# Kernel optimization log

Hardware: AMD Instinct MI355X
Metric: run time of the kernel (lower is better)

## Reference

```python
import jax, jax.numpy as jnp
import numpy as np

N_ATOMS = 2048
N_METAL = 512
BOX = (20.0, 20.0, 40.0)   # orthorhombic slab cell (A)
DL = 2.0                    # EwaldPotential dl -> k-grid half-extent per dim
SIGMA = 0.5540037           # 1/1.805132, Gaussian charge width
NMAX = tuple(int(np.ceil(L / DL)) for L in BOX)


def _kgrid():
    # integer reciprocal-lattice grid, k=0 excluded (built once at trace time)
    nx, ny, nz = NMAX
    g = np.stack(np.meshgrid(np.arange(-nx, nx + 1),
                             np.arange(-ny, ny + 1),
                             np.arange(-nz, nz + 1), indexing='ij'), -1).reshape(-1, 3)
    g = g[np.any(g != 0, axis=1)]
    return g.astype(np.float32)

_GRID = _kgrid()  # [K,3]


def ewald_field(r, q, cell):
    """Reciprocal-space Ewald potential phi_i = dE/dq_i for Gaussian-smeared charges.
    r:[N,3] q:[N,C] cell:[3,3] (rows = lattice vectors). Returns [N,C]."""
    V = jnp.abs(jnp.linalg.det(cell))
    recip = 2.0 * jnp.pi * jnp.linalg.inv(cell).T          # rows: reciprocal vectors
    k = jnp.asarray(_GRID, dtype=r.dtype) @ recip          # [K,3]
    k2 = jnp.sum(k * k, axis=-1)                           # [K]
    kfac = jnp.exp(-0.5 * SIGMA * SIGMA * k2) / k2         # exponent=1 kernel
    phase = r @ k.T                                        # [N,K]  (dominant traffic)
    c, s = jnp.cos(phase), jnp.sin(phase)
    cq = kfac[:, None] * (c.T @ q)                         # [K,C]
    sq = kfac[:, None] * (s.T @ q)
    return (4.0 * jnp.pi / V) * (c @ cq + s @ sq)          # [N,C]


def setup_inputs() -> dict:
    key = jax.random.key(0)
    k1, k2 = jax.random.split(key)
    box = jnp.asarray(BOX, dtype=jnp.float32)
    positions = jax.random.uniform(k1, (N_ATOMS, 3), dtype=jnp.float32) * box
    q = jax.random.normal(k2, (N_ATOMS, 1), dtype=jnp.float32) * 0.5
    cell = jnp.diag(box)
    # metal (Z=79) atoms occupy the first N_METAL slots; rest electrolyte (Z=8)
    atomic_numbers = jnp.concatenate([
        jnp.full((N_METAL,), 79, dtype=jnp.int32),
        jnp.full((N_ATOMS - N_METAL,), 8, dtype=jnp.int32)])
    return {"positions": positions, "q": q, "cell": cell,
            "atomic_numbers": atomic_numbers, "n_metal": N_METAL}


def reference(positions, q, cell, atomic_numbers, n_metal):
    nm = int(n_metal)  # static: metal atoms are the first nm rows
    dt = positions.dtype
    # q_all[metal] = 0
    q = q.at[:nm].set(0.0)
    # capacitance matrix S from detached coords (torch uses r.detach(), cell.detach())
    r_m = jax.lax.stop_gradient(positions[:nm])
    cell_d = jax.lax.stop_gradient(cell)
    A = ewald_field(r_m, jnp.eye(nm, dtype=dt), cell_d)     # [nm,nm] A_mat
    A_inv = jnp.linalg.inv(A)
    ones = jnp.ones((nm, 1), dtype=dt)
    Ai1 = A_inv @ ones                                       # [nm,1]
    S = A_inv - (Ai1 @ Ai1.T) / (ones.T @ Ai1)               # charge-neutral projector
    # full-system field; scaling_factor=1, external_field=None -> B_ext = 0
    f = ewald_field(positions, q, cell)                      # [N,1]
    B = -f[:nm]
    q_mw = q.at[:nm].set(S @ B)
    e_corr = jnp.zeros((1,), dtype=dt)   # scaling_factor == 1.0 branch
    e_ext = jnp.zeros((1,), dtype=dt)    # external_field is None
    return q_mw, e_corr, e_ext
```

## Files before the change

### kernel.cpp

```cpp
#include <hip/hip_runtime.h>
#include <math.h>

#define N_ATOMS 2048
#define NM      512
#define KHALF   9040
#define KPAD    9216
#define TWO_PI  6.2831853071795864769f
#define SIGMA   0.5540037f
#define FOUR_PI 12.566370614359172954f

__device__ inline void inv3x3(const float* __restrict__ c, float inv[3][3], float& det) {
    float a00=c[0],a01=c[1],a02=c[2],a10=c[3],a11=c[4],a12=c[5],a20=c[6],a21=c[7],a22=c[8];
    float c00 =  a11*a22 - a12*a21;
    float c01 = -(a10*a22 - a12*a20);
    float c02 =  a10*a21 - a11*a20;
    det = a00*c00 + a01*c01 + a02*c02;
    float id = 1.0f/det;
    inv[0][0] = c00*id;
    inv[0][1] = -(a01*a22 - a02*a21)*id;
    inv[0][2] =  (a01*a12 - a02*a11)*id;
    inv[1][0] = c01*id;
    inv[1][1] =  (a00*a22 - a02*a20)*id;
    inv[1][2] = -(a00*a12 - a02*a10)*id;
    inv[2][0] = c02*id;
// ... 22 lines not shown
                     float4* __restrict__ uq, float* __restrict__ out) {
    const int bb = blockIdx.x, tid = threadIdx.x;
    if (bb < 36) {
        int t = bb*256 + tid;
        float gx=0.f, gy=0.f, gz=0.f, wk=0.f;
        if (t < KHALF) {
            int iz = t % 41; int rem = t / 41; int iy = rem % 21; int ix = rem / 21;
            gx = (float)(ix - 10); gy = (float)(iy - 10); gz = (float)(iz - 20);
            float inv[3][3], det;
            inv3x3(cell, inv, det);
            float kx = TWO_PI*(gx*inv[0][0] + gy*inv[0][1] + gz*inv[0][2]);
            float ky = TWO_PI*(gx*inv[1][0] + gy*inv[1][1] + gz*inv[1][2]);
            float kz = TWO_PI*(gx*inv[2][0] + gy*inv[2][1] + gz*inv[2][2]);
            float k2 = kx*kx + ky*ky + kz*kz;
            float kfac = __expf(-0.5f*SIGMA*SIGMA*k2) / k2;
            wk = sqrtf(2.0f*kfac);
        }
        kdata[t] = make_float4(gx, gy, gz, wk);
    } else {
        int i = (bb-36)*256 + tid;
        float inv[3][3], det;
        inv3x3(cell, inv, det);
        float x = pos[3*i], y = pos[3*i+1], z = pos[3*i+2];
        float u = x*inv[0][0] + y*inv[1][0] + z*inv[2][0];
        float v = x*inv[0][1] + y*inv[1][1] + z*inv[2][1];
        float w = x*inv[0][2] + y*inv[1][2] + z*inv[2][2];
        float qi = qv[i];
        uq[i] = make_float4(u, v, w, qi);
        if (i >= NM) out[i] = qi;
        if (i == 0) { out[N_ATOMS] = 0.f; out[N_ATOMS+1] = 0.f; }
    }
}

__global__ void __launch_bounds__(256, 2) syrk_sf(const float4* __restrict__ kdata,
        const float4* __restrict__ uq, float* __restrict__ partial,
        float* __restrict__ Scw, float* __restrict__ Ssw, int SL, int KSL, int nsyrk) {
    __shared__ float smem[16384];
    const int tid = threadIdx.x;
    if ((int)blockIdx.x >= nsyrk) {
        int ch = blockIdx.x - nsyrk;
        int kk = tid & 63, sp = tid >> 6;
        int k = ch*64 + kk;
        float4 kd = kdata[k];
        float sc = 0.f, ss = 0.f;
        int jlo = NM + sp*384, jhi = jlo + 384;
        for (int j = jlo; j < jhi; ++j) {
            float4 at = uq[j];
            float ph = TWO_PI*(kd.x*at.x + kd.y*at.y + kd.z*at.z);
            float s, c; __sincosf(ph, &s, &c);
            sc += at.w * c;
            ss += at.w * s;
        }
        smem[sp*64 + kk] = sc;
        smem[256 + sp*64 + kk] = ss;
        __syncthreads();
        if (sp == 0) {
            float c = smem[kk] + smem[64+kk] + smem[128+kk] + smem[192+kk];
            float s = smem[256+kk] + smem[320+kk] + smem[384+kk] + smem[448+kk];
            float kf2 = kd.w * kd.w;
            Scw[k] = kf2 * c;
            Ssw[k] = kf2 * s;
        }
        return;
    }
    int s = blockIdx.x % SL;
    int t = blockIdx.x / SL;
    int rt = 0;
    while ((rt+1)*(rt+2)/2 <= t) ++rt;
    int ct = t - rt*(rt+1)/2;
    const int row0 = rt << 7, c0 = ct << 7;
    const bool diag = (row0 == c0);
    float* crT = smem; float* srT = smem+4096; float* ccT = smem+8192; float* scT = smem+12288;
    const float* ccR = diag ? crT : ccT;
    const float* scR = diag ? srT : scT;
    const int i0 = (tid & 15) << 3;
    const int j0 = (tid >> 4) << 3;
    float acc[8][8];
    #pragma unroll
    for (int i = 0; i < 8; ++i)
        #pragma unroll
        for (int j = 0; j < 8; ++j) acc[i][j] = 0.f;
    const int k0 = s * KSL;
    const int nch = KSL >> 5;
    for (int ch = 0; ch < nch; ++ch) {
        int kc = k0 + (ch << 5);
        __syncthreads();
        #pragma unroll
        for (int w = 0; w < 16; ++w) {
            int job = tid + (w << 8);
            int kk = job >> 7, a = job & 127;
            float4 kd = kdata[kc + kk];
            float4 at = uq[row0 + a];
            float ph = TWO_PI*(kd.x*at.x + kd.y*at.y + kd.z*at.z);
            float sn, cs;
            __sincosf(ph, &sn, &cs);
            crT[kk*128+a] = kd.w * cs;
            srT[kk*128+a] = kd.w * sn;
        }
        if (!diag) {
            #pragma unroll
            for (int w = 0; w < 16; ++w) {
                int job = tid + (w << 8);
                int kk = job >> 7, a = job & 127;
                float4 kd = kdata[kc + kk];
                float4 at = uq[c0 + a];
                float ph = TWO_PI*(kd.x*at.x + kd.y*at.y + kd.z*at.z);
                float sn, cs;
                __sincosf(ph, &sn, &cs);
                ccT[kk*128+a] = kd.w * cs;
                scT[kk*128+a] = kd.w * sn;
            }
        }
        __syncthreads();
        #pragma unroll 4
        for (int kk = 0; kk < 32; ++kk) {
            float cr[8], sr[8], cc[8], sv[8];
            *(float4*)&cr[0] = *(const float4*)&crT[kk*128+i0];
            *(float4*)&cr[4] = *(const float4*)&crT[kk*128+i0+4];
            *(float4*)&sr[0] = *(const float4*)&srT[kk*128+i0];
            *(float4*)&sr[4] = *(const float4*)&srT[kk*128+i0+4];
            *(float4*)&cc[0] = *(const float4*)&ccR[kk*128+j0];
            *(float4*)&cc[4] = *(const float4*)&ccR[kk*128+j0+4];
            *(float4*)&sv[0] = *(const float4*)&scR[kk*128+j0];
            *(float4*)&sv[4] = *(const float4*)&scR[kk*128+j0+4];
            #pragma unroll
            for (int i = 0; i < 8; ++i)
                #pragma unroll
                for (int j = 0; j < 8; ++j)
                    acc[i][j] += cr[i]*cc[j] + sr[i]*sv[j];
        }
    }
    float* P = partial + ((size_t)blockIdx.x << 14);
    #pragma unroll
    for (int i = 0; i < 8; ++i) {
        *(float4*)&P[(i0+i)*128 + j0]     = make_float4(acc[i][0], acc[i][1], acc[i][2], acc[i][3]);
        *(float4*)&P[(i0+i)*128 + j0 + 4] = make_float4(acc[i][4], acc[i][5], acc[i][6], acc[i][7]);
    }
}

__device__ void diag_fast(float* D, float* T, float* M, int tid, int pd, float* Dinvs) {
    __syncthreads();
    if (tid < 64) {
        float row[64];
        #pragma unroll
        for (int c = 0; c < 64; ++c) row[c] = D[tid*68 + c];
        #pragma unroll
        for (int j = 0; j < 64; ++j) {
            float pj = __shfl(row[j], j);
            float rinv = 1.0f / sqrtf(pj);
            float lj = row[j] * rinv;
            row[j] = lj;
            #pragma unroll
            for (int c = j+1; c < 64; ++c) {
                float lcj = __shfl(lj, c);
                row[c] = fmaf(-lj, lcj, row[c]);
            }
        }
        #pragma unroll
        for (int c = 0; c < 64; ++c) D[tid*68 + c] = row[c];
    }
    __syncthreads();
    for (int idx = tid; idx < 64*68; idx += 256) T[idx] = 0.f;
    __syncthreads();
    if (tid < 64) {
        int s = tid >> 3, c = tid & 7, o = s*8;
        float x[8];
        #pragma unroll
        for (int r = 0; r < 8; ++r) {
            float acc = (r == c) ? 1.0f : 0.0f;
// ... 67 lines not shown
                a0 += p[(size_t)(s+0) << 14];
                a1 += p[(size_t)(s+1) << 14];
                a2 += p[(size_t)(s+2) << 14];
                a3 += p[(size_t)(s+3) << 14];
                a4 += p[(size_t)(s+4) << 14];
                a5 += p[(size_t)(s+5) << 14];
                a6 += p[(size_t)(s+6) << 14];
                a7 += p[(size_t)(s+7) << 14];
            }
            for (; s < SL; ++s) a0 += p[(size_t)s << 14];
            float sum = ((a0+a1)+(a2+a3)) + ((a4+a5)+(a6+a7));
            float v = scal * sum;
            Amat[(size_t)i*512 + j] = v;
            Amat[(size_t)j*512 + i] = v;
        }
    } else {
        int ch = b - 512;
        int atom = ch*4 + (tid >> 6);
        int lane = tid & 63;
        float4 at = uq[atom];
        float acc = 0.f;
        for (int k = lane; k < KPAD; k += 64) {
            float4 kd = kdata[k];
            float ph = TWO_PI*(kd.x*at.x + kd.y*at.y + kd.z*at.z);
            float s, c; __sincosf(ph, &s, &c);
            acc += c*Scw[k] + s*Ssw[k];
        }
        #pragma unroll
        for (int off = 32; off; off >>= 1) acc += __shfl_down(acc, off);
        if (lane == 0) Bvec[atom] = -scal * acc;
    }
}

__global__ void __launch_bounds__(256) tail_chol(float* __restrict__ Amat,
        float* __restrict__ Lmat, float* __restrict__ LmatT, float* __restrict__ Dinvs,
        int* cnt, int* flag) {
    __shared__ float smem[15360];
    const int b = blockIdx.x, tid = threadIdx.x;
    const int G = 28;

    if (b == 0) {
        float* D = smem; float* T = smem + 4352; float* M = smem + 8704;
        for (int idx = tid; idx < 4096; idx += 256) {
            int r = idx >> 6, c = idx & 63;
            D[r*68+c] = Amat[(size_t)r*512 + c];
        }
        diag_fast(D, T, M, tid, 0, Dinvs);
    }
    gbar(cnt, flag, 1, G);

    for (int p = 0; p <= 6; ++p) {
        const int T7 = 7 - p, ntile = T7*(T7+1)/2;
        if (b < ntile) {
            const int tt = b;
            int rt = 0; while ((rt+1)*(rt+2)/2 <= tt) ++rt;
            const int ct = tt - rt*(rt+1)/2;
            const int R = p + 1 + rt, C = p + 1 + ct;
            float* ArT = smem;
            float* DvT = smem + 4352;
            float* LrT = smem + 8704;
            float* LcT = smem + 13056;
            float4 pref4[4];
            if (R != C) {
                #pragma unroll
                for (int w = 0; w < 4; ++w) {
                    int j = tid + (w << 8);
                    pref4[w] = *(const float4*)&Amat[(size_t)(C*64 + (j >> 4))*512 + p*64 + (j & 15)*4];
                }
            }
            __syncthreads();
            #pragma unroll
            for (int w = 0; w < 4; ++w) {
                int t4 = tid + (w << 8);
                float4 v = *(const float4*)&Dinvs[p*4096 + t4*4];
                int j = t4 >> 4, d0 = (t4 & 15)*4;
                DvT[(d0+0)*68 + j] = v.x;
                DvT[(d0+1)*68 + j] = v.y;
                DvT[(d0+2)*68 + j] = v.z;
                DvT[(d0+3)*68 + j] = v.w;
            }
            #pragma unroll
            for (int w = 0; w < 4; ++w) {
                int j = tid + (w << 8);
                int i = j >> 4, k0 = (j & 15)*4;
                float4 v = *(const float4*)&Amat[(size_t)(R*64 + i)*512 + p*64 + k0];
                ArT[(k0+0)*68 + i] = v.x;
                ArT[(k0+1)*68 + i] = v.y;
                ArT[(k0+2)*68 + i] = v.z;
                ArT[(k0+3)*68 + i] = v.w;
            }
            __syncthreads();
            const int i0 = (tid & 15)*4, j0 = (tid >> 4)*4;
            float lr[4][4];
            #pragma unroll
            for (int ii = 0; ii < 4; ++ii)
                #pragma unroll
                for (int jj = 0; jj < 4; ++jj) lr[ii][jj] = 0.f;
            for (int k = 0; k < 64; ++k) {
                float4 av = *(float4*)&ArT[k*68 + i0];
                float4 dv = *(float4*)&DvT[k*68 + j0];
                lr[0][0] += av.x*dv.x; lr[0][1] += av.x*dv.y; lr[0][2] += av.x*dv.z; lr[0][3] += av.x*dv.w;
                lr[1][0] += av.y*dv.x; lr[1][1] += av.y*dv.y; lr[1][2] += av.y*dv.z; lr[1][3] += av.y*dv.w;
                lr[2][0] += av.z*dv.x; lr[2][1] += av.z*dv.y; lr[2][2] += av.z*dv.z; lr[2][3] += av.z*dv.w;
                lr[3][0] += av.w*dv.x; lr[3][1] += av.w*dv.y; lr[3][2] += av.w*dv.z; lr[3][3] += av.w*dv.w;
            }
            #pragma unroll
            for (int ii = 0; ii < 4; ++ii)
                #pragma unroll
                for (int jj = 0; jj < 4; ++jj)
                    LrT[(j0+jj)*68 + i0+ii] = lr[ii][jj];
            __syncthreads();
            if (C == p + 1) {
                for (int idx = tid; idx < 4096; idx += 256) {
                    int i2 = idx >> 6, c2 = idx & 63;
                    Lmat[(size_t)(R*64+i2)*512 + p*64 + c2] = LrT[c2*68 + i2];
                }
                for (int idx = tid; idx < 4096; idx += 256) {
                    int c2 = idx >> 6, i2 = idx & 63;
                    LmatT[(size_t)(p*64+c2)*512 + R*64 + i2] = LrT[c2*68 + i2];
                }
            }
            if (R == C) {
                float up[4][4];
                #pragma unroll
                for (int ii = 0; ii < 4; ++ii)
                    #pragma unroll
                    for (int jj = 0; jj < 4; ++jj) up[ii][jj] = 0.f;
                for (int k = 0; k < 64; ++k) {
                    float4 av = *(float4*)&LrT[k*68 + i0];
                    float4 bv = *(float4*)&LrT[k*68 + j0];
                    up[0][0] += av.x*bv.x; up[0][1] += av.x*bv.y; up[0][2] += av.x*bv.z; up[0][3] += av.x*bv.w;
                    up[1][0] += av.y*bv.x; up[1][1] += av.y*bv.y; up[1][2] += av.y*bv.z; up[1][3] += av.y*bv.w;
                    up[2][0] += av.z*bv.x; up[2][1] += av.z*bv.y; up[2][2] += av.z*bv.z; up[2][3] += av.z*bv.w;
                    up[3][0] += av.w*bv.x; up[3][1] += av.w*bv.y; up[3][2] += av.w*bv.z; up[3][3] += av.w*bv.w;
                }
                float vals[4][4];
                #pragma unroll
                for (int ii = 0; ii < 4; ++ii)
                    #pragma unroll
                    for (int jj = 0; jj < 4; ++jj) {
                        size_t gix = (size_t)(R*64+i0+ii)*512 + C*64 + j0 + jj;
                        float v = Amat[gix] - up[ii][jj];
                        Amat[gix] = v;
                        vals[ii][jj] = v;
                    }
                if (tt == 0) {
                    float* D = smem; float* T = smem + 4352; float* M = smem + 8704;
                    __syncthreads();
                    #pragma unroll
                    for (int ii = 0; ii < 4; ++ii)
                        #pragma unroll
                        for (int jj = 0; jj < 4; ++jj)
                            D[(i0+ii)*68 + j0+jj] = vals[ii][jj];
                    diag_fast(D, T, M, tid, p+1, Dinvs);
                }
            } else {
                #pragma unroll
                for (int w = 0; w < 4; ++w) {
                    int j = tid + (w << 8);
                    int i = j >> 4, k0 = (j & 15)*4;
                    ArT[(k0+0)*68 + i] = pref4[w].x;
                    ArT[(k0+1)*68 + i] = pref4[w].y;
                    ArT[(k0+2)*68 + i] = pref4[w].z;
                    ArT[(k0+3)*68 + i] = pref4[w].w;
                }
                __syncthreads();
                const int c0l = (tid & 15)*4, jr0 = (tid >> 4)*2;
                #pragma unroll
                for (int hh = 0; hh < 2; ++hh) {
                    float lc[4][2];
                    #pragma unroll
                    for (int cc = 0; cc < 4; ++cc) { lc[cc][0] = 0.f; lc[cc][1] = 0.f; }
                    for (int d = 0; d < 64; ++d) {
                        float4 dv = *(float4*)&DvT[d*68 + c0l];
                        float2 av = *(float2*)&ArT[d*68 + hh*32 + jr0];
                        lc[0][0] += dv.x*av.x; lc[0][1] += dv.x*av.y;
                        lc[1][0] += dv.y*av.x; lc[1][1] += dv.y*av.y;
                        lc[2][0] += dv.z*av.x; lc[2][1] += dv.z*av.y;
                        lc[3][0] += dv.w*av.x; lc[3][1] += dv.w*av.y;
                    }
                    __syncthreads();
                    #pragma unroll
                    for (int cc = 0; cc < 4; ++cc) {
                        LcT[(c0l+cc)*36 + jr0]     = lc[cc][0];
                        LcT[(c0l+cc)*36 + jr0 + 1] = lc[cc][1];
                    }
                    __syncthreads();
                    float up[4][2];
                    #pragma unroll
                    for (int ii = 0; ii < 4; ++ii) { up[ii][0] = 0.f; up[ii][1] = 0.f; }
                    for (int c2 = 0; c2 < 64; ++c2) {
                        float4 lv = *(float4*)&LrT[c2*68 + i0];
                        float2 cv = *(float2*)&LcT[c2*36 + jr0];
                        up[0][0] += lv.x*cv.x; up[0][1] += lv.x*cv.y;
                        up[1][0] += lv.y*cv.x; up[1][1] += lv.y*cv.y;
                        up[2][0] += lv.z*cv.x; up[2][1] += lv.z*cv.y;
                        up[3][0] += lv.w*cv.x; up[3][1] += lv.w*cv.y;
                    }
                    #pragma unroll
                    for (int ii = 0; ii < 4; ++ii)
                        #pragma unroll
                        for (int jr = 0; jr < 2; ++jr) {
                            size_t gix = (size_t)(R*64+i0+ii)*512 + C*64 + hh*32 + jr0 + jr;
                            Amat[gix] -= up[ii][jr];
                        }
                }
            }
        }
        if (p < 6) gbar(cnt, flag, p + 2, G);
    }
}

__global__ void __launch_bounds__(512) solve(const float* __restrict__ Lmat,
        const float* __restrict__ LmatT, const float* __restrict__ Dinvs,
        const float* __restrict__ Bvec, float* __restrict__ out) {
    __shared__ float smem[2592];
    float* rb  = smem;
    float* ro  = smem + 512;
    float* xb  = smem + 1024;
    float* xo  = smem + 1536;
    float* bvs = smem + 2048;
    float* red = smem + 2560;
    const int tid = threadIdx.x;
    if (tid < 512) {
        float bv = Bvec[tid];
        bvs[tid] = bv; rb[tid] = bv; ro[tid] = 1.0f;
    }
    __syncthreads();
    for (int k = 0; k < 8; ++k) {
        if (tid < 64) {
            const float* Dk = Dinvs + k*4096 + tid*64;
            float s1 = 0.f, s2 = 0.f;
            for (int c4 = 0; c4 < 16; ++c4) {
                float4 w = *(const float4*)&Dk[c4*4];
                int cb = 64*k + c4*4;
                s1 += w.x*rb[cb] + w.y*rb[cb+1] + w.z*rb[cb+2] + w.w*rb[cb+3];
                s2 += w.x*ro[cb] + w.y*ro[cb+1] + w.z*ro[cb+2] + w.w*ro[cb+3];
            }
            rb[64*k+tid] = s1; ro[64*k+tid] = s2;
        }
        __syncthreads();
        for (int mm = 64*(k+1) + tid; mm < 512; mm += 512) {
// ... 44 lines not shown
        #pragma unroll
        for (int i = 0; i < 8; ++i) { sn += red[i]; sd += red[16+i]; }
        red[31] = sn / sd;
    }
    __syncthreads();
    float ratio = red[31];
    if (tid < 512) out[tid] = xb[tid] - xo[tid]*ratio;
}

extern "C" void kernel_launch(void* const* d_in, const int* in_sizes, int n_in,
                              void* d_out, int out_size, void* d_ws, size_t ws_size,
                              hipStream_t stream) {
    (void)in_sizes; (void)n_in; (void)out_size;
    const float* pos  = (const float*)d_in[0];
    const float* qv   = (const float*)d_in[1];
    const float* cell = (const float*)d_in[2];
    float* out = (float*)d_out;
    char* ws = (char*)d_ws;
    size_t off = 0;
    auto alloc = [&](size_t bytes) -> void* {
        void* p = (void*)(ws + off);
        off = (off + bytes + 255) & ~(size_t)255;
        return p;
    };
    float4* kdata = (float4*)alloc((size_t)KPAD*16);
    float4* uq    = (float4*)alloc((size_t)N_ATOMS*16);
    float*  Scw   = (float*)alloc((size_t)KPAD*4);
    float*  Ssw   = (float*)alloc((size_t)KPAD*4);
    float*  Bvec  = (float*)alloc(512*4);
    float*  Amat  = (float*)alloc((size_t)512*512*4);
    float*  Lmat  = (float*)alloc((size_t)512*512*4);
    float*  LmatT = (float*)alloc((size_t)512*512*4);
    float*  Dinvs = (float*)alloc((size_t)8*4096*4);
    int* bar = (int*)alloc(256);
    static const int slopts[10] = {96, 72, 48, 36, 24, 16, 12, 8, 4, 1};
    int SL = 1;
    for (int ci = 0; ci < 10; ++ci) {
        size_t need = (size_t)10 * slopts[ci] * 16384 * 4;
        if (off + need <= ws_size) { SL = slopts[ci]; break; }
    }
    float* partial = (float*)alloc((size_t)10*SL*16384*4);
    const int KSL = KPAD / SL;
    const int nsyrk = 10*SL;

    hipMemsetAsync(bar, 0, 8, stream);
    prep<<<dim3(44), dim3(256), 0, stream>>>(pos, qv, cell, kdata, uq, out);
    syrk_sf<<<dim3(nsyrk + 144), dim3(256), 0, stream>>>(kdata, uq, partial,
                                                         Scw, Ssw, SL, KSL, nsyrk);
    redfield<<<dim3(640), dim3(256), 0, stream>>>(partial, cell, Amat, kdata, uq,
                                                  Scw, Ssw, Bvec, SL);
    tail_chol<<<dim3(28), dim3(256), 0, stream>>>(Amat, Lmat, LmatT, Dinvs,
                                                  bar, bar + 1);
    solve<<<dim3(1), dim3(512), 0, stream>>>(Lmat, LmatT, Dinvs, Bvec, out);
}
```

Measured before the change: 537.5 us.

## Serialize last Cholesky panels in one block and interleave GEMM thread tiles

The per-tile Cholesky update is factored into a helper. The blocked Cholesky now runs only the first four panel steps across the cooperative grid with global barriers. The last three steps, which have few tiles, run sequentially in block 0 after a single arrival counter, so several grid-wide barriers are removed in exchange for serial work on one block. Separately, the Ewald GEMM thread mapping changes from contiguous 8x8 sub-tiles to two 4-wide groups strided by 64, which is meant to reduce LDS bank conflicts on the float4 loads.

```diff
diff --git a/kernel.cpp b/kernel.cpp
--- a/kernel.cpp
+++ b/kernel.cpp
@@ -119,8 +119,8 @@
     float* crT = smem; float* srT = smem+4096; float* ccT = smem+8192; float* scT = smem+12288;
     const float* ccR = diag ? crT : ccT;
     const float* scR = diag ? srT : scT;
-    const int i0 = (tid & 15) << 3;
-    const int j0 = (tid >> 4) << 3;
+    const int i0 = (tid & 15) << 2;
+    const int j0 = (tid >> 4) << 2;
     float acc[8][8];
     #pragma unroll
     for (int i = 0; i < 8; ++i)
@@ -160,15 +160,18 @@
         __syncthreads();
         #pragma unroll 4
         for (int kk = 0; kk < 32; ++kk) {
-            float cr[8], sr[8], cc[8], sv[8];
-            *(float4*)&cr[0] = *(const float4*)&crT[kk*128+i0];
-            *(float4*)&cr[4] = *(const float4*)&crT[kk*128+i0+4];
-            *(float4*)&sr[0] = *(const float4*)&srT[kk*128+i0];
-            *(float4*)&sr[4] = *(const float4*)&srT[kk*128+i0+4];
-            *(float4*)&cc[0] = *(const float4*)&ccR[kk*128+j0];
-            *(float4*)&cc[4] = *(const float4*)&ccR[kk*128+j0+4];
-            *(float4*)&sv[0] = *(const float4*)&scR[kk*128+j0];
-            *(float4*)&sv[4] = *(const float4*)&scR[kk*128+j0+4];
+            float4 c0v = *(const float4*)&crT[kk*128+i0];
+            float4 c1v = *(const float4*)&crT[kk*128+i0+64];
+            float4 s0v = *(const float4*)&srT[kk*128+i0];
+            float4 s1v = *(const float4*)&srT[kk*128+i0+64];
+            float4 d0v = *(const float4*)&ccR[kk*128+j0];
+            float4 d1v = *(const float4*)&ccR[kk*128+j0+64];
+            float4 t0v = *(const float4*)&scR[kk*128+j0];
+            float4 t1v = *(const float4*)&scR[kk*128+j0+64];
+            float cr[8] = {c0v.x,c0v.y,c0v.z,c0v.w, c1v.x,c1v.y,c1v.z,c1v.w};
+            float sr[8] = {s0v.x,s0v.y,s0v.z,s0v.w, s1v.x,s1v.y,s1v.z,s1v.w};
+            float cc[8] = {d0v.x,d0v.y,d0v.z,d0v.w, d1v.x,d1v.y,d1v.z,d1v.w};
+            float sv[8] = {t0v.x,t0v.y,t0v.z,t0v.w, t1v.x,t1v.y,t1v.z,t1v.w};
             #pragma unroll
             for (int i = 0; i < 8; ++i)
                 #pragma unroll
@@ -179,8 +182,9 @@
     float* P = partial + ((size_t)blockIdx.x << 14);
     #pragma unroll
     for (int i = 0; i < 8; ++i) {
-        *(float4*)&P[(i0+i)*128 + j0]     = make_float4(acc[i][0], acc[i][1], acc[i][2], acc[i][3]);
-        *(float4*)&P[(i0+i)*128 + j0 + 4] = make_float4(acc[i][4], acc[i][5], acc[i][6], acc[i][7]);
+        int row = (i < 4) ? (i0 + i) : (64 + i0 + i - 4);
+        *(float4*)&P[row*128 + j0]      = make_float4(acc[i][0], acc[i][1], acc[i][2], acc[i][3]);
+        *(float4*)&P[row*128 + j0 + 64] = make_float4(acc[i][4], acc[i][5], acc[i][6], acc[i][7]);
     }
 }
 
@@ -314,6 +318,163 @@
     }
 }
 
+__device__ void chol_tile(float* Amat, float* Lmat, float* LmatT, float* Dinvs,
+                          float* smem, int tid, int p, int tt) {
+    int rt = 0; while ((rt+1)*(rt+2)/2 <= tt) ++rt;
+    const int ct = tt - rt*(rt+1)/2;
+    const int R = p + 1 + rt, C = p + 1 + ct;
+    float* ArT = smem;
+    float* DvT = smem + 4352;
+    float* LrT = smem + 8704;
+    float* LcT = smem + 13056;
+    float4 pref4[4];
+    if (R != C) {
+        #pragma unroll
+        for (int w = 0; w < 4; ++w) {
+            int j = tid + (w << 8);
+            pref4[w] = *(const float4*)&Amat[(size_t)(C*64 + (j >> 4))*512 + p*64 + (j & 15)*4];
+        }
+    }
+    __syncthreads();
+    #pragma unroll
+    for (int w = 0; w < 4; ++w) {
+        int t4 = tid + (w << 8);
+        float4 v = *(const float4*)&Dinvs[p*4096 + t4*4];
+        int j = t4 >> 4, d0 = (t4 & 15)*4;
+        DvT[(d0+0)*68 + j] = v.x;
+        DvT[(d0+1)*68 + j] = v.y;
+        DvT[(d0+2)*68 + j] = v.z;
+        DvT[(d0+3)*68 + j] = v.w;
+    }
+    #pragma unroll
+    for (int w = 0; w < 4; ++w) {
+        int j = tid + (w << 8);
+        int i = j >> 4, k0 = (j & 15)*4;
+        float4 v = *(const float4*)&Amat[(size_t)(R*64 + i)*512 + p*64 + k0];
+        ArT[(k0+0)*68 + i] = v.x;
+        ArT[(k0+1)*68 + i] = v.y;
+        ArT[(k0+2)*68 + i] = v.z;
+        ArT[(k0+3)*68 + i] = v.w;
+    }
+    __syncthreads();
+    const int i0 = (tid & 15)*4, j0 = (tid >> 4)*4;
+    float lr[4][4];
+    #pragma unroll
+    for (int ii = 0; ii < 4; ++ii)
+        #pragma unroll
+        for (int jj = 0; jj < 4; ++jj) lr[ii][jj] = 0.f;
+    for (int k = 0; k < 64; ++k) {
+        float4 av = *(float4*)&ArT[k*68 + i0];
+        float4 dv = *(float4*)&DvT[k*68 + j0];
+        lr[0][0] += av.x*dv.x; lr[0][1] += av.x*dv.y; lr[0][2] += av.x*dv.z; lr[0][3] += av.x*dv.w;
+        lr[1][0] += av.y*dv.x; lr[1][1] += av.y*dv.y; lr[1][2] += av.y*dv.z; lr[1][3] += av.y*dv.w;
+        lr[2][0] += av.z*dv.x; lr[2][1] += av.z*dv.y; lr[2][2] += av.z*dv.z; lr[2][3] += av.z*dv.w;
+        lr[3][0] += av.w*dv.x; lr[3][1] += av.w*dv.y; lr[3][2] += av.w*dv.z; lr[3][3] += av.w*dv.w;
+    }
+    #pragma unroll
+    for (int ii = 0; ii < 4; ++ii)
+        #pragma unroll
+        for (int jj = 0; jj < 4; ++jj)
+            LrT[(j0+jj)*68 + i0+ii] = lr[ii][jj];
+    __syncthreads();
+    if (C == p + 1) {
+        for (int idx = tid; idx < 4096; idx += 256) {
+            int i2 = idx >> 6, c2 = idx & 63;
+            Lmat[(size_t)(R*64+i2)*512 + p*64 + c2] = LrT[c2*68 + i2];
+        }
+        for (int idx = tid; idx < 4096; idx += 256) {
+            int c2 = idx >> 6, i2 = idx & 63;
+            LmatT[(size_t)(p*64+c2)*512 + R*64 + i2] = LrT[c2*68 + i2];
+        }
+    }
+    if (R == C) {
+        float up[4][4];
+        #pragma unroll
+        for (int ii = 0; ii < 4; ++ii)
+            #pragma unroll
+            for (int jj = 0; jj < 4; ++jj) up[ii][jj] = 0.f;
+        for (int k = 0; k < 64; ++k) {
+            float4 av = *(float4*)&LrT[k*68 + i0];
+            float4 bv = *(float4*)&LrT[k*68 + j0];
+            up[0][0] += av.x*bv.x; up[0][1] += av.x*bv.y; up[0][2] += av.x*bv.z; up[0][3] += av.x*bv.w;
+            up[1][0] += av.y*bv.x; up[1][1] += av.y*bv.y; up[1][2] += av.y*bv.z; up[1][3] += av.y*bv.w;
+            up[2][0] += av.z*bv.x; up[2][1] += av.z*bv.y; up[2][2] += av.z*bv.z; up[2][3] += av.z*bv.w;
+            up[3][0] += av.w*bv.x; up[3][1] += av.w*bv.y; up[3][2] += av.w*bv.z; up[3][3] += av.w*bv.w;
+        }
+        float vals[4][4];
+        #pragma unroll
+        for (int ii = 0; ii < 4; ++ii)
+            #pragma unroll
+            for (int jj = 0; jj < 4; ++jj) {
+                size_t gix = (size_t)(R*64+i0+ii)*512 + C*64 + j0 + jj;
+                float v = Amat[gix] - up[ii][jj];
+                Amat[gix] = v;
+                vals[ii][jj] = v;
+            }
+        if (tt == 0) {
+            float* D = smem; float* T = smem + 4352; float* M = smem + 8704;
+            __syncthreads();
+            #pragma unroll
+            for (int ii = 0; ii < 4; ++ii)
+                #pragma unroll
+                for (int jj = 0; jj < 4; ++jj)
+                    D[(i0+ii)*68 + j0+jj] = vals[ii][jj];
+            diag_fast(D, T, M, tid, p+1, Dinvs);
+        }
+    } else {
+        #pragma unroll
+        for (int w = 0; w < 4; ++w) {
+            int j = tid + (w << 8);
+            int i = j >> 4, k0 = (j & 15)*4;
+            ArT[(k0+0)*68 + i] = pref4[w].x;
+            ArT[(k0+1)*68 + i] = pref4[w].y;
+            ArT[(k0+2)*68 + i] = pref4[w].z;
+            ArT[(k0+3)*68 + i] = pref4[w].w;
+        }
+        __syncthreads();
+        const int c0l = (tid & 15)*4, jr0 = (tid >> 4)*2;
+        #pragma unroll
+        for (int hh = 0; hh < 2; ++hh) {
+            float lc[4][2];
+            #pragma unroll
+            for (int cc = 0; cc < 4; ++cc) { lc[cc][0] = 0.f; lc[cc][1] = 0.f; }
+            for (int d = 0; d < 64; ++d) {
+                float4 dv = *(float4*)&DvT[d*68 + c0l];
+                float2 av = *(float2*)&ArT[d*68 + hh*32 + jr0];
+                lc[0][0] += dv.x*av.x; lc[0][1] += dv.x*av.y;
+                lc[1][0] += dv.y*av.x; lc[1][1] += dv.y*av.y;
+                lc[2][0] += dv.z*av.x; lc[2][1] += dv.z*av.y;
+                lc[3][0] += dv.w*av.x; lc[3][1] += dv.w*av.y;
+            }
+            __syncthreads();
+            #pragma unroll
+            for (int cc = 0; cc < 4; ++cc) {
+                LcT[(c0l+cc)*36 + jr0]     = lc[cc][0];
+                LcT[(c0l+cc)*36 + jr0 + 1] = lc[cc][1];
+            }
+            __syncthreads();
+            float up[4][2];
+            #pragma unroll
+            for (int ii = 0; ii < 4; ++ii) { up[ii][0] = 0.f; up[ii][1] = 0.f; }
+            for (int c2 = 0; c2 < 64; ++c2) {
+                float4 lv = *(float4*)&LrT[c2*68 + i0];
+                float2 cv = *(float2*)&LcT[c2*36 + jr0];
+                up[0][0] += lv.x*cv.x; up[0][1] += lv.x*cv.y;
+                up[1][0] += lv.y*cv.x; up[1][1] += lv.y*cv.y;
+                up[2][0] += lv.z*cv.x; up[2][1] += lv.z*cv.y;
+                up[3][0] += lv.w*cv.x; up[3][1] += lv.w*cv.y;
+            }
+            #pragma unroll
+            for (int ii = 0; ii < 4; ++ii)
+                #pragma unroll
+                for (int jr = 0; jr < 2; ++jr) {
+                    size_t gix = (size_t)(R*64+i0+ii)*512 + C*64 + hh*32 + jr0 + jr;
+                    Amat[gix] -= up[ii][jr];
+                }
+        }
+    }
+}
+
 __global__ void __launch_bounds__(256) tail_chol(float* __restrict__ Amat,
         float* __restrict__ Lmat, float* __restrict__ LmatT, float* __restrict__ Dinvs,
         int* cnt, int* flag) {
@@ -331,165 +492,25 @@
     }
     gbar(cnt, flag, 1, G);
 
-    for (int p = 0; p <= 6; ++p) {
+    for (int p = 0; p <= 3; ++p) {
         const int T7 = 7 - p, ntile = T7*(T7+1)/2;
-        if (b < ntile) {
-            const int tt = b;
-            int rt = 0; while ((rt+1)*(rt+2)/2 <= tt) ++rt;
-            const int ct = tt - rt*(rt+1)/2;
-            const int R = p + 1 + rt, C = p + 1 + ct;
-            float* ArT = smem;
-            float* DvT = smem + 4352;
-            float* LrT = smem + 8704;
-            float* LcT = smem + 13056;
-            float4 pref4[4];
-            if (R != C) {
-                #pragma unroll
-                for (int w = 0; w < 4; ++w) {
-                    int j = tid + (w << 8);
-                    pref4[w] = *(const float4*)&Amat[(size_t)(C*64 + (j >> 4))*512 + p*64 + (j & 15)*4];
-                }
-            }
-            __syncthreads();
-            #pragma unroll
-            for (int w = 0; w < 4; ++w) {
-                int t4 = tid + (w << 8);
-                float4 v = *(const float4*)&Dinvs[p*4096 + t4*4];
-                int j = t4 >> 4, d0 = (t4 & 15)*4;
-                DvT[(d0+0)*68 + j] = v.x;
-                DvT[(d0+1)*68 + j] = v.y;
-                DvT[(d0+2)*68 + j] = v.z;
-                DvT[(d0+3)*68 + j] = v.w;
-            }
-            #pragma unroll
-            for (int w = 0; w < 4; ++w) {
-                int j = tid + (w << 8);
-                int i = j >> 4, k0 = (j & 15)*4;
-                float4 v = *(const float4*)&Amat[(size_t)(R*64 + i)*512 + p*64 + k0];
-                ArT[(k0+0)*68 + i] = v.x;
-                ArT[(k0+1)*68 + i] = v.y;
-                ArT[(k0+2)*68 + i] = v.z;
-                ArT[(k0+3)*68 + i] = v.w;
-            }
-            __syncthreads();
-            const int i0 = (tid & 15)*4, j0 = (tid >> 4)*4;
-            float lr[4][4];
-            #pragma unroll
-            for (int ii = 0; ii < 4; ++ii)
-                #pragma unroll
-                for (int jj = 0; jj < 4; ++jj) lr[ii][jj] = 0.f;
-            for (int k = 0; k < 64; ++k) {
-                float4 av = *(float4*)&ArT[k*68 + i0];
-                float4 dv = *(float4*)&DvT[k*68 + j0];
-                lr[0][0] += av.x*dv.x; lr[0][1] += av.x*dv.y; lr[0][2] += av.x*dv.z; lr[0][3] += av.x*dv.w;
-                lr[1][0] += av.y*dv.x; lr[1][1] += av.y*dv.y; lr[1][2] += av.y*dv.z; lr[1][3] += av.y*dv.w;
-                lr[2][0] += av.z*dv.x; lr[2][1] += av.z*dv.y; lr[2][2] += av.z*dv.z; lr[2][3] += av.z*dv.w;
-                lr[3][0] += av.w*dv.x; lr[3][1] += av.w*dv.y; lr[3][2] += av.w*dv.z; lr[3][3] += av.w*dv.w;
-            }
-            #pragma unroll
-            for (int ii = 0; ii < 4; ++ii)
-                #pragma unroll
-                for (int jj = 0; jj < 4; ++jj)
-                    LrT[(j0+jj)*68 + i0+ii] = lr[ii][jj];
-            __syncthreads();
-            if (C == p + 1) {
-                for (int idx = tid; idx < 4096; idx += 256) {
-                    int i2 = idx >> 6, c2 = idx & 63;
-                    Lmat[(size_t)(R*64+i2)*512 + p*64 + c2] = LrT[c2*68 + i2];
-                }
-                for (int idx = tid; idx < 4096; idx += 256) {
-                    int c2 = idx >> 6, i2 = idx & 63;
-                    LmatT[(size_t)(p*64+c2)*512 + R*64 + i2] = LrT[c2*68 + i2];
-                }
-            }
-            if (R == C) {
-                float up[4][4];
-                #pragma unroll
-                for (int ii = 0; ii < 4; ++ii)
-                    #pragma unroll
-                    for (int jj = 0; jj < 4; ++jj) up[ii][jj] = 0.f;
-                for (int k = 0; k < 64; ++k) {
-                    float4 av = *(float4*)&LrT[k*68 + i0];
-                    float4 bv = *(float4*)&LrT[k*68 + j0];
-                    up[0][0] += av.x*bv.x; up[0][1] += av.x*bv.y; up[0][2] += av.x*bv.z; up[0][3] += av.x*bv.w;
-                    up[1][0] += av.y*bv.x; up[1][1] += av.y*bv.y; up[1][2] += av.y*bv.z; up[1][3] += av.y*bv.w;
-                    up[2][0] += av.z*bv.x; up[2][1] += av.z*bv.y; up[2][2] += av.z*bv.z; up[2][3] += av.z*bv.w;
-                    up[3][0] += av.w*bv.x; up[3][1] += av.w*bv.y; up[3][2] += av.w*bv.z; up[3][3] += av.w*bv.w;
-                }
-                float vals[4][4];
-                #pragma unroll
-                for (int ii = 0; ii < 4; ++ii)
-                    #pragma unroll
-                    for (int jj = 0; jj < 4; ++jj) {
-                        size_t gix = (size_t)(R*64+i0+ii)*512 + C*64 + j0 + jj;
-                        float v = Amat[gix] - up[ii][jj];
-                        Amat[gix] = v;
-                        vals[ii][jj] = v;
-                    }
-                if (tt == 0) {
-                    float* D = smem; float* T = smem + 4352; float* M = smem + 8704;
-                    __syncthreads();
-                    #pragma unroll
-                    for (int ii = 0; ii < 4; ++ii)
-                        #pragma unroll
-                        for (int jj = 0; jj < 4; ++jj)
-                            D[(i0+ii)*68 + j0+jj] = vals[ii][jj];
-                    diag_fast(D, T, M, tid, p+1, Dinvs);
-                }
-            } else {
-                #pragma unroll
-                for (int w = 0; w < 4; ++w) {
-                    int j = tid + (w << 8);
-                    int i = j >> 4, k0 = (j & 15)*4;
-                    ArT[(k0+0)*68 + i] = pref4[w].x;
-                    ArT[(k0+1)*68 + i] = pref4[w].y;
-                    ArT[(k0+2)*68 + i] = pref4[w].z;
-                    ArT[(k0+3)*68 + i] = pref4[w].w;
-                }
-                __syncthreads();
-                const int c0l = (tid & 15)*4, jr0 = (tid >> 4)*2;
-                #pragma unroll
-                for (int hh = 0; hh < 2; ++hh) {
-                    float lc[4][2];
-                    #pragma unroll
-                    for (int cc = 0; cc < 4; ++cc) { lc[cc][0] = 0.f; lc[cc][1] = 0.f; }
-                    for (int d = 0; d < 64; ++d) {
-                        float4 dv = *(float4*)&DvT[d*68 + c0l];
-                        float2 av = *(float2*)&ArT[d*68 + hh*32 + jr0];
-                        lc[0][0] += dv.x*av.x; lc[0][1] += dv.x*av.y;
-                        lc[1][0] += dv.y*av.x; lc[1][1] += dv.y*av.y;
-                        lc[2][0] += dv.z*av.x; lc[2][1] += dv.z*av.y;
-                        lc[3][0] += dv.w*av.x; lc[3][1] += dv.w*av.y;
-                    }
-                    __syncthreads();
-                    #pragma unroll
-                    for (int cc = 0; cc < 4; ++cc) {
-                        LcT[(c0l+cc)*36 + jr0]     = lc[cc][0];
-                        LcT[(c0l+cc)*36 + jr0 + 1] = lc[cc][1];
-                    }
-                    __syncthreads();
-                    float up[4][2];
-                    #pragma unroll
-                    for (int ii = 0; ii < 4; ++ii) { up[ii][0] = 0.f; up[ii][1] = 0.f; }
-                    for (int c2 = 0; c2 < 64; ++c2) {
-                        float4 lv = *(float4*)&LrT[c2*68 + i0];
-                        float2 cv = *(float2*)&LcT[c2*36 + jr0];
-                        up[0][0] += lv.x*cv.x; up[0][1] += lv.x*cv.y;
-                        up[1][0] += lv.y*cv.x; up[1][1] += lv.y*cv.y;
-                        up[2][0] += lv.z*cv.x; up[2][1] += lv.z*cv.y;
-                        up[3][0] += lv.w*cv.x; up[3][1] += lv.w*cv.y;
-                    }
-                    #pragma unroll
-                    for (int ii = 0; ii < 4; ++ii)
-                        #pragma unroll
-                        for (int jr = 0; jr < 2; ++jr) {
-                            size_t gix = (size_t)(R*64+i0+ii)*512 + C*64 + hh*32 + jr0 + jr;
-                            Amat[gix] -= up[ii][jr];
-                        }
-                }
-            }
-        }
-        if (p < 6) gbar(cnt, flag, p + 2, G);
+        if (b < ntile) chol_tile(Amat, Lmat, LmatT, Dinvs, smem, tid, p, b);
+        if (p < 3) gbar(cnt, flag, p + 2, G);
+    }
+    __syncthreads();
+    if (tid == 0)
+        __hip_atomic_fetch_add(cnt, 1, __ATOMIC_RELEASE, __HIP_MEMORY_SCOPE_AGENT);
+    if (b != 0) return;
+    if (tid == 0) {
+        while (__hip_atomic_load(cnt, __ATOMIC_RELAXED, __HIP_MEMORY_SCOPE_AGENT) < G*5)
+            __builtin_amdgcn_s_sleep(2);
+        (void)__hip_atomic_load(cnt, __ATOMIC_ACQUIRE, __HIP_MEMORY_SCOPE_AGENT);
+    }
+    __syncthreads();
+    for (int p = 4; p <= 6; ++p) {
+        const int T7 = 7 - p, ntile = T7*(T7+1)/2;
+        for (int tt = 0; tt < ntile; ++tt)
+            chol_tile(Amat, Lmat, LmatT, Dinvs, smem, tid, p, tt);
     }
 }
 
```

Measured after the change: 631.9 us. 17.6% more time.

## Precompute weighted cos/sin table once instead of recomputing per SYRK tile

Applied to the files above, without the earlier changes.

Adds a kernel that writes a weighted cos/sin table of shape [K,512] for the metal atoms into two ~19 MB global buffers. The SYRK blocks then load their tiles from this table with float4 loads instead of recomputing sincos for every (row, column) tile pair, which removes redundant transcendental work repeated across the 10 tile pairs. In exchange it adds about 38 MB of write and read traffic, and the workspace gets smaller, which may force a lower SL split. The Cholesky tile body is also moved into a device function with no change in behaviour.

```diff
diff --git a/kernel.cpp b/kernel.cpp
--- a/kernel.cpp
+++ b/kernel.cpp
@@ -78,8 +78,40 @@
     }
 }
 
+__global__ void __launch_bounds__(256) tabk(const float4* __restrict__ kdata,
+        const float4* __restrict__ uq, float* __restrict__ Tc, float* __restrict__ Ts) {
+    int e = blockIdx.x*256 + threadIdx.x;
+    int k = e >> 7;
+    int a0 = (e & 127) << 2;
+    float4 kd = kdata[k];
+    float4 cs4, sn4;
+    {
+        float4 at = uq[a0+0];
+        float ph = TWO_PI*(kd.x*at.x + kd.y*at.y + kd.z*at.z);
+        float s, c; __sincosf(ph, &s, &c); cs4.x = kd.w*c; sn4.x = kd.w*s;
+    }
+    {
+        float4 at = uq[a0+1];
+        float ph = TWO_PI*(kd.x*at.x + kd.y*at.y + kd.z*at.z);
+        float s, c; __sincosf(ph, &s, &c); cs4.y = kd.w*c; sn4.y = kd.w*s;
+    }
+    {
+        float4 at = uq[a0+2];
+        float ph = TWO_PI*(kd.x*at.x + kd.y*at.y + kd.z*at.z);
+        float s, c; __sincosf(ph, &s, &c); cs4.z = kd.w*c; sn4.z = kd.w*s;
+    }
+    {
+        float4 at = uq[a0+3];
+        float ph = TWO_PI*(kd.x*at.x + kd.y*at.y + kd.z*at.z);
+        float s, c; __sincosf(ph, &s, &c); cs4.w = kd.w*c; sn4.w = kd.w*s;
+    }
+    *(float4*)&Tc[(size_t)k*512 + a0] = cs4;
+    *(float4*)&Ts[(size_t)k*512 + a0] = sn4;
+}
+
 __global__ void __launch_bounds__(256, 2) syrk_sf(const float4* __restrict__ kdata,
-        const float4* __restrict__ uq, float* __restrict__ partial,
+        const float4* __restrict__ uq, const float* __restrict__ Tc,
+        const float* __restrict__ Ts, float* __restrict__ partial,
         float* __restrict__ Scw, float* __restrict__ Ssw, int SL, int KSL, int nsyrk) {
     __shared__ float smem[16384];
     const int tid = threadIdx.x;
@@ -132,29 +164,21 @@
         int kc = k0 + (ch << 5);
         __syncthreads();
         #pragma unroll
-        for (int w = 0; w < 16; ++w) {
-            int job = tid + (w << 8);
-            int kk = job >> 7, a = job & 127;
-            float4 kd = kdata[kc + kk];
-            float4 at = uq[row0 + a];
-            float ph = TWO_PI*(kd.x*at.x + kd.y*at.y + kd.z*at.z);
-            float sn, cs;
-            __sincosf(ph, &sn, &cs);
-            crT[kk*128+a] = kd.w * cs;
-            srT[kk*128+a] = kd.w * sn;
+        for (int w = 0; w < 4; ++w) {
+            int e = tid + (w << 8);
+            int kk = e >> 5, a4 = (e & 31) << 2;
+            size_t gix = (size_t)(kc + kk)*512 + row0 + a4;
+            *(float4*)&crT[kk*128 + a4] = *(const float4*)&Tc[gix];
+            *(float4*)&srT[kk*128 + a4] = *(const float4*)&Ts[gix];
         }
         if (!diag) {
             #pragma unroll
-            for (int w = 0; w < 16; ++w) {
-                int job = tid + (w << 8);
-                int kk = job >> 7, a = job & 127;
-                float4 kd = kdata[kc + kk];
-                float4 at = uq[c0 + a];
-                float ph = TWO_PI*(kd.x*at.x + kd.y*at.y + kd.z*at.z);
-                float sn, cs;
-                __sincosf(ph, &sn, &cs);
-                ccT[kk*128+a] = kd.w * cs;
-                scT[kk*128+a] = kd.w * sn;
+            for (int w = 0; w < 4; ++w) {
+                int e = tid + (w << 8);
+                int kk = e >> 5, a4 = (e & 31) << 2;
+                size_t gix = (size_t)(kc + kk)*512 + c0 + a4;
+                *(float4*)&ccT[kk*128 + a4] = *(const float4*)&Tc[gix];
+                *(float4*)&scT[kk*128 + a4] = *(const float4*)&Ts[gix];
             }
         }
         __syncthreads();
@@ -314,6 +338,163 @@
     }
 }
 
+__device__ void chol_tile(float* Amat, float* Lmat, float* LmatT, float* Dinvs,
+                          float* smem, int tid, int p, int tt) {
+    int rt = 0; while ((rt+1)*(rt+2)/2 <= tt) ++rt;
+    const int ct = tt - rt*(rt+1)/2;
+    const int R = p + 1 + rt, C = p + 1 + ct;
+    float* ArT = smem;
+    float* DvT = smem + 4352;
+    float* LrT = smem + 8704;
+    float* LcT = smem + 13056;
+    float4 pref4[4];
+    if (R != C) {
+        #pragma unroll
+        for (int w = 0; w < 4; ++w) {
+            int j = tid + (w << 8);
+            pref4[w] = *(const float4*)&Amat[(size_t)(C*64 + (j >> 4))*512 + p*64 + (j & 15)*4];
+        }
+    }
+    __syncthreads();
+    #pragma unroll
+    for (int w = 0; w < 4; ++w) {
+        int t4 = tid + (w << 8);
+        float4 v = *(const float4*)&Dinvs[p*4096 + t4*4];
+        int j = t4 >> 4, d0 = (t4 & 15)*4;
+        DvT[(d0+0)*68 + j] = v.x;
+        DvT[(d0+1)*68 + j] = v.y;
+        DvT[(d0+2)*68 + j] = v.z;
+        DvT[(d0+3)*68 + j] = v.w;
+    }
+    #pragma unroll
+    for (int w = 0; w < 4; ++w) {
+        int j = tid + (w << 8);
+        int i = j >> 4, k0 = (j & 15)*4;
+        float4 v = *(const float4*)&Amat[(size_t)(R*64 + i)*512 + p*64 + k0];
+        ArT[(k0+0)*68 + i] = v.x;
+        ArT[(k0+1)*68 + i] = v.y;
+        ArT[(k0+2)*68 + i] = v.z;
+        ArT[(k0+3)*68 + i] = v.w;
+    }
+    __syncthreads();
+    const int i0 = (tid & 15)*4, j0 = (tid >> 4)*4;
+    float lr[4][4];
+    #pragma unroll
+    for (int ii = 0; ii < 4; ++ii)
+        #pragma unroll
+        for (int jj = 0; jj < 4; ++jj) lr[ii][jj] = 0.f;
+    for (int k = 0; k < 64; ++k) {
+        float4 av = *(float4*)&ArT[k*68 + i0];
+        float4 dv = *(float4*)&DvT[k*68 + j0];
+        lr[0][0] += av.x*dv.x; lr[0][1] += av.x*dv.y; lr[0][2] += av.x*dv.z; lr[0][3] += av.x*dv.w;
+        lr[1][0] += av.y*dv.x; lr[1][1] += av.y*dv.y; lr[1][2] += av.y*dv.z; lr[1][3] += av.y*dv.w;
+        lr[2][0] += av.z*dv.x; lr[2][1] += av.z*dv.y; lr[2][2] += av.z*dv.z; lr[2][3] += av.z*dv.w;
+        lr[3][0] += av.w*dv.x; lr[3][1] += av.w*dv.y; lr[3][2] += av.w*dv.z; lr[3][3] += av.w*dv.w;
+    }
+    #pragma unroll
+    for (int ii = 0; ii < 4; ++ii)
+        #pragma unroll
+        for (int jj = 0; jj < 4; ++jj)
+            LrT[(j0+jj)*68 + i0+ii] = lr[ii][jj];
+    __syncthreads();
+    if (C == p + 1) {
+        for (int idx = tid; idx < 4096; idx += 256) {
+            int i2 = idx >> 6, c2 = idx & 63;
+            Lmat[(size_t)(R*64+i2)*512 + p*64 + c2] = LrT[c2*68 + i2];
+        }
+        for (int idx = tid; idx < 4096; idx += 256) {
+            int c2 = idx >> 6, i2 = idx & 63;
+            LmatT[(size_t)(p*64+c2)*512 + R*64 + i2] = LrT[c2*68 + i2];
+        }
+    }
+    if (R == C) {
+        float up[4][4];
+        #pragma unroll
+        for (int ii = 0; ii < 4; ++ii)
+            #pragma unroll
+            for (int jj = 0; jj < 4; ++jj) up[ii][jj] = 0.f;
+        for (int k = 0; k < 64; ++k) {
+            float4 av = *(float4*)&LrT[k*68 + i0];
+            float4 bv = *(float4*)&LrT[k*68 + j0];
+            up[0][0] += av.x*bv.x; up[0][1] += av.x*bv.y; up[0][2] += av.x*bv.z; up[0][3] += av.x*bv.w;
+            up[1][0] += av.y*bv.x; up[1][1] += av.y*bv.y; up[1][2] += av.y*bv.z; up[1][3] += av.y*bv.w;
+            up[2][0] += av.z*bv.x; up[2][1] += av.z*bv.y; up[2][2] += av.z*bv.z; up[2][3] += av.z*bv.w;
+            up[3][0] += av.w*bv.x; up[3][1] += av.w*bv.y; up[3][2] += av.w*bv.z; up[3][3] += av.w*bv.w;
+        }
+        float vals[4][4];
+        #pragma unroll
+        for (int ii = 0; ii < 4; ++ii)
+            #pragma unroll
+            for (int jj = 0; jj < 4; ++jj) {
+                size_t gix = (size_t)(R*64+i0+ii)*512 + C*64 + j0 + jj;
+                float v = Amat[gix] - up[ii][jj];
+                Amat[gix] = v;
+                vals[ii][jj] = v;
+            }
+        if (tt == 0) {
+            float* D = smem; float* T = smem + 4352; float* M = smem + 8704;
+            __syncthreads();
+            #pragma unroll
+            for (int ii = 0; ii < 4; ++ii)
+                #pragma unroll
+                for (int jj = 0; jj < 4; ++jj)
+                    D[(i0+ii)*68 + j0+jj] = vals[ii][jj];
+            diag_fast(D, T, M, tid, p+1, Dinvs);
+        }
+    } else {
+        #pragma unroll
+        for (int w = 0; w < 4; ++w) {
+            int j = tid + (w << 8);
+            int i = j >> 4, k0 = (j & 15)*4;
+            ArT[(k0+0)*68 + i] = pref4[w].x;
+            ArT[(k0+1)*68 + i] = pref4[w].y;
+            ArT[(k0+2)*68 + i] = pref4[w].z;
+            ArT[(k0+3)*68 + i] = pref4[w].w;
+        }
+        __syncthreads();
+        const int c0l = (tid & 15)*4, jr0 = (tid >> 4)*2;
+        #pragma unroll
+        for (int hh = 0; hh < 2; ++hh) {
+            float lc[4][2];
+            #pragma unroll
+            for (int cc = 0; cc < 4; ++cc) { lc[cc][0] = 0.f; lc[cc][1] = 0.f; }
+            for (int d = 0; d < 64; ++d) {
+                float4 dv = *(float4*)&DvT[d*68 + c0l];
+                float2 av = *(float2*)&ArT[d*68 + hh*32 + jr0];
+                lc[0][0] += dv.x*av.x; lc[0][1] += dv.x*av.y;
+                lc[1][0] += dv.y*av.x; lc[1][1] += dv.y*av.y;
+                lc[2][0] += dv.z*av.x; lc[2][1] += dv.z*av.y;
+                lc[3][0] += dv.w*av.x; lc[3][1] += dv.w*av.y;
+            }
+            __syncthreads();
+            #pragma unroll
+            for (int cc = 0; cc < 4; ++cc) {
+                LcT[(c0l+cc)*36 + jr0]     = lc[cc][0];
+                LcT[(c0l+cc)*36 + jr0 + 1] = lc[cc][1];
+            }
+            __syncthreads();
+            float up[4][2];
+            #pragma unroll
+            for (int ii = 0; ii < 4; ++ii) { up[ii][0] = 0.f; up[ii][1] = 0.f; }
+            for (int c2 = 0; c2 < 64; ++c2) {
+                float4 lv = *(float4*)&LrT[c2*68 + i0];
+                float2 cv = *(float2*)&LcT[c2*36 + jr0];
+                up[0][0] += lv.x*cv.x; up[0][1] += lv.x*cv.y;
+                up[1][0] += lv.y*cv.x; up[1][1] += lv.y*cv.y;
+                up[2][0] += lv.z*cv.x; up[2][1] += lv.z*cv.y;
+                up[3][0] += lv.w*cv.x; up[3][1] += lv.w*cv.y;
+            }
+            #pragma unroll
+            for (int ii = 0; ii < 4; ++ii)
+                #pragma unroll
+                for (int jr = 0; jr < 2; ++jr) {
+                    size_t gix = (size_t)(R*64+i0+ii)*512 + C*64 + hh*32 + jr0 + jr;
+                    Amat[gix] -= up[ii][jr];
+                }
+        }
+    }
+}
+
 __global__ void __launch_bounds__(256) tail_chol(float* __restrict__ Amat,
         float* __restrict__ Lmat, float* __restrict__ LmatT, float* __restrict__ Dinvs,
         int* cnt, int* flag) {
@@ -333,162 +514,7 @@
 
     for (int p = 0; p <= 6; ++p) {
         const int T7 = 7 - p, ntile = T7*(T7+1)/2;
-        if (b < ntile) {
-            const int tt = b;
-            int rt = 0; while ((rt+1)*(rt+2)/2 <= tt) ++rt;
-            const int ct = tt - rt*(rt+1)/2;
-            const int R = p + 1 + rt, C = p + 1 + ct;
-            float* ArT = smem;
-            float* DvT = smem + 4352;
-            float* LrT = smem + 8704;
-            float* LcT = smem + 13056;
-            float4 pref4[4];
-            if (R != C) {
-                #pragma unroll
-                for (int w = 0; w < 4; ++w) {
-                    int j = tid + (w << 8);
-                    pref4[w] = *(const float4*)&Amat[(size_t)(C*64 + (j >> 4))*512 + p*64 + (j & 15)*4];
-                }
-            }
-            __syncthreads();
-            #pragma unroll
-            for (int w = 0; w < 4; ++w) {
-                int t4 = tid + (w << 8);
-                float4 v = *(const float4*)&Dinvs[p*4096 + t4*4];
-                int j = t4 >> 4, d0 = (t4 & 15)*4;
-                DvT[(d0+0)*68 + j] = v.x;
-                DvT[(d0+1)*68 + j] = v.y;
-                DvT[(d0+2)*68 + j] = v.z;
-                DvT[(d0+3)*68 + j] = v.w;
-            }
-            #pragma unroll
-            for (int w = 0; w < 4; ++w) {
-                int j = tid + (w << 8);
-                int i = j >> 4, k0 = (j & 15)*4;
-                float4 v = *(const float4*)&Amat[(size_t)(R*64 + i)*512 + p*64 + k0];
-                ArT[(k0+0)*68 + i] = v.x;
-                ArT[(k0+1)*68 + i] = v.y;
-                ArT[(k0+2)*68 + i] = v.z;
-                ArT[(k0+3)*68 + i] = v.w;
-            }
-            __syncthreads();
-            const int i0 = (tid & 15)*4, j0 = (tid >> 4)*4;
-            float lr[4][4];
-            #pragma unroll
-            for (int ii = 0; ii < 4; ++ii)
-                #pragma unroll
-                for (int jj = 0; jj < 4; ++jj) lr[ii][jj] = 0.f;
-            for (int k = 0; k < 64; ++k) {
-                float4 av = *(float4*)&ArT[k*68 + i0];
-                float4 dv = *(float4*)&DvT[k*68 + j0];
-                lr[0][0] += av.x*dv.x; lr[0][1] += av.x*dv.y; lr[0][2] += av.x*dv.z; lr[0][3] += av.x*dv.w;
-                lr[1][0] += av.y*dv.x; lr[1][1] += av.y*dv.y; lr[1][2] += av.y*dv.z; lr[1][3] += av.y*dv.w;
-                lr[2][0] += av.z*dv.x; lr[2][1] += av.z*dv.y; lr[2][2] += av.z*dv.z; lr[2][3] += av.z*dv.w;
-                lr[3][0] += av.w*dv.x; lr[3][1] += av.w*dv.y; lr[3][2] += av.w*dv.z; lr[3][3] += av.w*dv.w;
-            }
-            #pragma unroll
-            for (int ii = 0; ii < 4; ++ii)
-                #pragma unroll
-                for (int jj = 0; jj < 4; ++jj)
-                    LrT[(j0+jj)*68 + i0+ii] = lr[ii][jj];
-            __syncthreads();
-            if (C == p + 1) {
-                for (int idx = tid; idx < 4096; idx += 256) {
-                    int i2 = idx >> 6, c2 = idx & 63;
-                    Lmat[(size_t)(R*64+i2)*512 + p*64 + c2] = LrT[c2*68 + i2];
-                }
-                for (int idx = tid; idx < 4096; idx += 256) {
-                    int c2 = idx >> 6, i2 = idx & 63;
-                    LmatT[(size_t)(p*64+c2)*512 + R*64 + i2] = LrT[c2*68 + i2];
-                }
-            }
-            if (R == C) {
-                float up[4][4];
-                #pragma unroll
-                for (int ii = 0; ii < 4; ++ii)
-                    #pragma unroll
-                    for (int jj = 0; jj < 4; ++jj) up[ii][jj] = 0.f;
-                for (int k = 0; k < 64; ++k) {
-                    float4 av = *(float4*)&LrT[k*68 + i0];
-                    float4 bv = *(float4*)&LrT[k*68 + j0];
-                    up[0][0] += av.x*bv.x; up[0][1] += av.x*bv.y; up[0][2] += av.x*bv.z; up[0][3] += av.x*bv.w;
-                    up[1][0] += av.y*bv.x; up[1][1] += av.y*bv.y; up[1][2] += av.y*bv.z; up[1][3] += av.y*bv.w;
-                    up[2][0] += av.z*bv.x; up[2][1] += av.z*bv.y; up[2][2] += av.z*bv.z; up[2][3] += av.z*bv.w;
-                    up[3][0] += av.w*bv.x; up[3][1] += av.w*bv.y; up[3][2] += av.w*bv.z; up[3][3] += av.w*bv.w;
-                }
-                float vals[4][4];
-                #pragma unroll
-                for (int ii = 0; ii < 4; ++ii)
-                    #pragma unroll
-                    for (int jj = 0; jj < 4; ++jj) {
-                        size_t gix = (size_t)(R*64+i0+ii)*512 + C*64 + j0 + jj;
-                        float v = Amat[gix] - up[ii][jj];
-                        Amat[gix] = v;
-                        vals[ii][jj] = v;
-                    }
-                if (tt == 0) {
-                    float* D = smem; float* T = smem + 4352; float* M = smem + 8704;
-                    __syncthreads();
-                    #pragma unroll
-                    for (int ii = 0; ii < 4; ++ii)
-                        #pragma unroll
-                        for (int jj = 0; jj < 4; ++jj)
-                            D[(i0+ii)*68 + j0+jj] = vals[ii][jj];
-                    diag_fast(D, T, M, tid, p+1, Dinvs);
-                }
-            } else {
-                #pragma unroll
-                for (int w = 0; w < 4; ++w) {
-                    int j = tid + (w << 8);
-                    int i = j >> 4, k0 = (j & 15)*4;
-                    ArT[(k0+0)*68 + i] = pref4[w].x;
-                    ArT[(k0+1)*68 + i] = pref4[w].y;
-                    ArT[(k0+2)*68 + i] = pref4[w].z;
-                    ArT[(k0+3)*68 + i] = pref4[w].w;
-                }
-                __syncthreads();
-                const int c0l = (tid & 15)*4, jr0 = (tid >> 4)*2;
-                #pragma unroll
-                for (int hh = 0; hh < 2; ++hh) {
-                    float lc[4][2];
-                    #pragma unroll
-                    for (int cc = 0; cc < 4; ++cc) { lc[cc][0] = 0.f; lc[cc][1] = 0.f; }
-                    for (int d = 0; d < 64; ++d) {
-                        float4 dv = *(float4*)&DvT[d*68 + c0l];
-                        float2 av = *(float2*)&ArT[d*68 + hh*32 + jr0];
-                        lc[0][0] += dv.x*av.x; lc[0][1] += dv.x*av.y;
-                        lc[1][0] += dv.y*av.x; lc[1][1] += dv.y*av.y;
-                        lc[2][0] += dv.z*av.x; lc[2][1] += dv.z*av.y;
-                        lc[3][0] += dv.w*av.x; lc[3][1] += dv.w*av.y;
-                    }
-                    __syncthreads();
-                    #pragma unroll
-                    for (int cc = 0; cc < 4; ++cc) {
-                        LcT[(c0l+cc)*36 + jr0]     = lc[cc][0];
-                        LcT[(c0l+cc)*36 + jr0 + 1] = lc[cc][1];
-                    }
-                    __syncthreads();
-                    float up[4][2];
-                    #pragma unroll
-                    for (int ii = 0; ii < 4; ++ii) { up[ii][0] = 0.f; up[ii][1] = 0.f; }
-                    for (int c2 = 0; c2 < 64; ++c2) {
-                        float4 lv = *(float4*)&LrT[c2*68 + i0];
-                        float2 cv = *(float2*)&LcT[c2*36 + jr0];
-                        up[0][0] += lv.x*cv.x; up[0][1] += lv.x*cv.y;
-                        up[1][0] += lv.y*cv.x; up[1][1] += lv.y*cv.y;
-                        up[2][0] += lv.z*cv.x; up[2][1] += lv.z*cv.y;
-                        up[3][0] += lv.w*cv.x; up[3][1] += lv.w*cv.y;
-                    }
-                    #pragma unroll
-                    for (int ii = 0; ii < 4; ++ii)
-                        #pragma unroll
-                        for (int jr = 0; jr < 2; ++jr) {
-                            size_t gix = (size_t)(R*64+i0+ii)*512 + C*64 + hh*32 + jr0 + jr;
-                            Amat[gix] -= up[ii][jr];
-                        }
-                }
-            }
-        }
+        if (b < ntile) chol_tile(Amat, Lmat, LmatT, Dinvs, smem, tid, p, b);
         if (p < 6) gbar(cnt, flag, p + 2, G);
     }
 }
@@ -600,6 +626,8 @@
     float*  Lmat  = (float*)alloc((size_t)512*512*4);
     float*  LmatT = (float*)alloc((size_t)512*512*4);
     float*  Dinvs = (float*)alloc((size_t)8*4096*4);
+    float*  Tc    = (float*)alloc((size_t)KPAD*512*4);
+    float*  Ts    = (float*)alloc((size_t)KPAD*512*4);
     int* bar = (int*)alloc(256);
     static const int slopts[10] = {96, 72, 48, 36, 24, 16, 12, 8, 4, 1};
     int SL = 1;
@@ -613,7 +641,8 @@
 
     hipMemsetAsync(bar, 0, 8, stream);
     prep<<<dim3(44), dim3(256), 0, stream>>>(pos, qv, cell, kdata, uq, out);
-    syrk_sf<<<dim3(nsyrk + 144), dim3(256), 0, stream>>>(kdata, uq, partial,
+    tabk<<<dim3(KPAD*128/256), dim3(256), 0, stream>>>(kdata, uq, Tc, Ts);
+    syrk_sf<<<dim3(nsyrk + 144), dim3(256), 0, stream>>>(kdata, uq, Tc, Ts, partial,
                                                          Scw, Ssw, SL, KSL, nsyrk);
     redfield<<<dim3(640), dim3(256), 0, stream>>>(partial, cell, Amat, kdata, uq,
                                                   Scw, Ssw, Bvec, SL);
```

Result: slower. 565.1 us (+5.1%).
